# Kernel tuning notes

Measured on AMD Instinct MI355X. Metric: run time of the kernel, lower is better.

## Reference

```python
import jax, jax.numpy as jnp
import numpy as np
import itertools

B, N, K, G = 1024, 1024, 6, 720  # G = K!
H1, H2, C = 64, 32, 40
IN = K * 3


def setup_inputs() -> dict:
    key = jax.random.key(0)
    ks = jax.random.split(key, 8)
    x = jax.random.normal(ks[0], (B, N, 3), dtype=jnp.float32)
    # per-sample subsample indices (torch uses randperm(N)[:K]; distinctness
    # is irrelevant to the math, randint keeps them in-range)
    idx = jax.random.randint(ks[1], (B, K), 0, N)
    perms = jnp.asarray(
        np.array(list(itertools.permutations(range(K))), dtype=np.int32)
    )  # (G, K)
    # MLP params: torch Linear default init ~ U(-1/sqrt(fan_in), 1/sqrt(fan_in))
    def lin(k, fin, fout):
        kw, kb = jax.random.split(k)
        s = 1.0 / np.sqrt(fin)
        W = jax.random.uniform(kw, (fin, fout), jnp.float32, -s, s)
        b = jax.random.uniform(kb, (fout,), jnp.float32, -s, s)
        return W, b
    W1, b1 = lin(ks[2], IN, H1)
    W2, b2 = lin(ks[3], H1, H2)
    W3, b3 = lin(ks[4], H2, C)
    return dict(x=x, W1=W1, b1=b1, W2=W2, b2=b2, W3=W3, b3=b3,
                idx=idx, perms=perms)


def reference(x, W1, b1, W2, b2, W3, b3, idx, perms):
    Bv = x.shape[0]
    Gv, Kv = perms.shape
    # gather the K subsampled points per batch element: (B, K, 3)
    pts = jnp.take_along_axis(x, idx[:, :, None], axis=1)
    # expand over all K! permutations of the point ordering: (B, G, K, 3)
    permuted = pts[:, perms, :]
    flat = permuted.reshape(Bv, Gv, Kv * 3)  # (B, G, K*3)
    h = jax.nn.relu(flat @ W1 + b1)          # (B, G, H1)
    h = jax.nn.relu(h @ W2 + b2)             # (B, G, H2)
    y = h @ W3 + b3                          # (B, G, C)
    return y.mean(axis=1)                    # (B, C)
```

## Files before the change

kernel.cpp:

```cpp
#include <hip/hip_runtime.h>
#include <hip/hip_bf16.h>

typedef __attribute__((ext_vector_type(8))) short short8;
typedef __attribute__((ext_vector_type(4))) float f32x4;
typedef __attribute__((ext_vector_type(4))) unsigned int u32x4;
typedef __attribute__((ext_vector_type(2))) unsigned int u32x2;

#define NN 1024

#define LFENCE { asm volatile("s_waitcnt lgkmcnt(0)" ::: "memory"); __builtin_amdgcn_sched_barrier(0); }

#define ROW_W(BUF, ROW, VAL) { \
  float v_ = fmaxf((VAL), 0.0f); \
  __hip_bfloat16 hb_ = __float2bfloat16(v_); \
  BUF[((ROW) * 64) + (lane ^ ((((ROW)) & 7) << 3))] = *(short*)&hb_; \
}

#define ROW6(BUF, R, BX) \
  ROW_W(BUF,(R)+0,(BX)+T0_) ROW_W(BUF,(R)+1,(BX)+T1_) ROW_W(BUF,(R)+2,(BX)+T2_) \
  ROW_W(BUF,(R)+3,(BX)+T3_) ROW_W(BUF,(R)+4,(BX)+T4_) ROW_W(BUF,(R)+5,(BX)+T5_)

#define SGR(BUF, A0,A1,A2, M0,M1,M2) do { \
  const float f0_ = b1v + P[(A0)*6+0]; \
  const float f1_ = b1v + P[(A1)*6+0]; \
  const float f2_ = b1v + P[(A2)*6+0]; \
  const float g12_ = P[(A1)*6+1] + P[(A2)*6+2]; \
  const float g21_ = P[(A2)*6+1] + P[(A1)*6+2]; \
  const float g02_ = P[(A0)*6+1] + P[(A2)*6+2]; \
  const float g20_ = P[(A2)*6+1] + P[(A0)*6+2]; \
  const float g01_ = P[(A0)*6+1] + P[(A1)*6+2]; \
  const float g10_ = P[(A1)*6+1] + P[(A0)*6+2]; \
  const float e0_ = P[(M0)*6+3], e1_ = P[(M1)*6+3], e2_ = P[(M2)*6+3]; \
  const float h12_ = P[(M1)*6+4] + P[(M2)*6+5]; \
  const float h21_ = P[(M2)*6+4] + P[(M1)*6+5]; \
  const float h02_ = P[(M0)*6+4] + P[(M2)*6+5]; \
  const float h20_ = P[(M2)*6+4] + P[(M0)*6+5]; \
  const float h01_ = P[(M0)*6+4] + P[(M1)*6+5]; \
  const float h10_ = P[(M1)*6+4] + P[(M0)*6+5]; \
  const float T0_ = e0_+h12_, T1_ = e0_+h21_, T2_ = e1_+h02_; \
  const float T3_ = e1_+h20_, T4_ = e2_+h01_, T5_ = e2_+h10_; \
  const float B0_ = f0_+g12_, B1_ = f0_+g21_, B2_ = f1_+g02_; \
  const float B3_ = f1_+g20_, B4_ = f2_+g01_, B5_ = f2_+g10_; \
  ROW6(BUF, 0,  B0_) ROW6(BUF, 6,  B1_) ROW6(BUF, 12, B2_) \
  ROW6(BUF, 18, B3_) ROW6(BUF, 24, B4_) ROW6(BUF, 30, B5_) \
} while(0)

#define MFMA4T(A0_, A1_) do { \
  f32x4 c0_ = {b2v0,b2v0,b2v0,b2v0}; \
  f32x4 c1_ = {b2v1,b2v1,b2v1,b2v1}; \
  c0_ = __builtin_amdgcn_mfma_f32_16x16x32_bf16(A0_, bh00, c0_, 0,0,0); \
  c0_ = __builtin_amdgcn_mfma_f32_16x16x32_bf16(A1_, bh10, c0_, 0,0,0); \
  c1_ = __builtin_amdgcn_mfma_f32_16x16x32_bf16(A0_, bh01, c1_, 0,0,0); \
  c1_ = __builtin_amdgcn_mfma_f32_16x16x32_bf16(A1_, bh11, c1_, 0,0,0); \
  acc0[0]+=fmaxf(c0_[0],0.f); acc0[1]+=fmaxf(c0_[1],0.f); \
  acc0[2]+=fmaxf(c0_[2],0.f); acc0[3]+=fmaxf(c0_[3],0.f); \
  acc1[0]+=fmaxf(c1_[0],0.f); acc1[1]+=fmaxf(c1_[1],0.f); \
  acc1[2]+=fmaxf(c1_[2],0.f); acc1[3]+=fmaxf(c1_[3],0.f); \
} while(0)

#define READS(BUF) { \
  r0 = *(const short8*)&BUF[0*1024 + e0i]; r1 = *(const short8*)&BUF[0*1024 + e1i]; \
  r2 = *(const short8*)&BUF[1*1024 + e0i]; r3 = *(const short8*)&BUF[1*1024 + e1i]; \
  r4 = *(const short8*)&BUF[2*1024 + e0i]; r5 = *(const short8*)&BUF[2*1024 + e1i]; }

#define MFMA3 { MFMA4T(r0,r1); MFMA4T(r2,r3); MFMA4T(r4,r5); }

#define CHUNK(BUF, A0,A1,A2, M0,M1,M2) { SGR(BUF, A0,A1,A2, M0,M1,M2); READS(BUF); LFENCE; }

#define ALLCHUNKS \
    if (wv == 0) { \
        CHUNK(wb0, 0,1,2, 3,4,5); \
        MFMA3; CHUNK(wb1, 0,1,3, 2,4,5); \
        MFMA3; CHUNK(wb0, 0,1,4, 2,3,5); \
        MFMA3; CHUNK(wb1, 0,1,5, 2,3,4); \
        MFMA3; CHUNK(wb0, 0,2,3, 1,4,5); \
        MFMA3; \
    } else if (wv == 1) { \
        CHUNK(wb0, 0,2,4, 1,3,5); \
        MFMA3; CHUNK(wb1, 0,2,5, 1,3,4); \
        MFMA3; CHUNK(wb0, 0,3,4, 1,2,5); \
        MFMA3; CHUNK(wb1, 0,3,5, 1,2,4); \
        MFMA3; CHUNK(wb0, 0,4,5, 1,2,3); \
        MFMA3; \
    } else if (wv == 2) { \
        CHUNK(wb0, 1,2,3, 0,4,5); \
        MFMA3; CHUNK(wb1, 1,2,4, 0,3,5); \
        MFMA3; CHUNK(wb0, 1,2,5, 0,3,4); \
        MFMA3; CHUNK(wb1, 1,3,4, 0,2,5); \
        MFMA3; CHUNK(wb0, 1,3,5, 0,2,4); \
        MFMA3; \
    } else { \
        CHUNK(wb0, 1,4,5, 0,2,3); \
        MFMA3; CHUNK(wb1, 2,3,4, 0,1,5); \
        MFMA3; CHUNK(wb0, 2,3,5, 0,1,4); \
        MFMA3; CHUNK(wb1, 2,4,5, 0,1,3); \
        MFMA3; CHUNK(wb0, 3,4,5, 0,1,2); \
        MFMA3; \
    }

#define MKB(dst_h, KH, NIDX) do { \
  _Pragma("unroll") \
  for (int e_ = 0; e_ < 8; ++e_) { \
    float f_ = W2[((KH)*32 + kg*8 + e_)*32 + 16*(NIDX) + colb]; \
    __hip_bfloat16 hi_ = __float2bfloat16(f_); \
    dst_h[e_] = *(short*)&hi_; \
  } \
} while(0)

__global__ __launch_bounds__(256, 2) void symm_mlp_kernel(
    const float* __restrict__ x,
    const float* __restrict__ W1, const float* __restrict__ b1,
    const float* __restrict__ W2, const float* __restrict__ b2,
    const float* __restrict__ W3, const float* __restrict__ b3,
    const int* __restrict__ idx,
    float* __restrict__ out)
{
    __shared__ short h1s[4][2][48 * 64];
    __shared__ float redbuf[4][32];

    const int tid   = threadIdx.x;
    const int lane  = tid & 63;
    const int wv    = tid >> 6;
    const int b0    = blockIdx.x * 2;

    int pidx0[6], pidx1[6];
    #pragma unroll
    for (int k = 0; k < 6; ++k) { pidx0[k] = idx[b0 * 6 + k]; pidx1[k] = idx[(b0 + 1) * 6 + k]; }

    float px0[6][3], px1[6][3];
    #pragma unroll
    for (int k = 0; k < 6; ++k)
        #pragma unroll
        for (int d = 0; d < 3; ++d) {
            px0[k][d] = x[(b0 * NN + pidx0[k]) * 3 + d];
            px1[k][d] = x[((b0 + 1) * NN + pidx1[k]) * 3 + d];
        }

    float w1c[18];
    #pragma unroll
    for (int r = 0; r < 18; ++r) w1c[r] = W1[r * 64 + lane];

    const float b1v = b1[lane];
    const int colb = lane & 15, kg = lane >> 4;
    const float b2v0 = b2[colb];
    const float b2v1 = b2[16 + colb];

    short8 bh00, bh10, bh01, bh11;
    MKB(bh00, 0, 0);
    MKB(bh10, 1, 0);
    MKB(bh01, 0, 1);
    MKB(bh11, 1, 1);

    short* wb0 = &h1s[wv][0][0];
    short* wb1 = &h1s[wv][1][0];
    *reinterpret_cast<u32x4*>(&wb0[2304 + lane * 8]) = u32x4{0u,0u,0u,0u};
    *reinterpret_cast<u32x2*>(&wb0[2816 + lane * 4]) = u32x2{0u,0u};
    *reinterpret_cast<u32x4*>(&wb1[2304 + lane * 8]) = u32x4{0u,0u,0u,0u};
    *reinterpret_cast<u32x2*>(&wb1[2816 + lane * 4]) = u32x2{0u,0u};

    const int Xl  = (lane & 7) << 3;
    const int e0i = (lane & 15) * 64 + ((kg * 8) ^ Xl);
    const int e1i = (lane & 15) * 64 + ((32 + kg * 8) ^ Xl);

    short8 r0, r1, r2, r3, r4, r5;

    #pragma unroll 1
    for (int bi = 0; bi < 2; ++bi) {
        float P[36];
        #pragma unroll
        for (int k = 0; k < 6; ++k) {
            const float x0 = bi ? px1[k][0] : px0[k][0];
            const float x1 = bi ? px1[k][1] : px0[k][1];
            const float x2 = bi ? px1[k][2] : px0[k][2];
            #pragma unroll
            for (int j = 0; j < 6; ++j)
                P[k*6+j] = fmaf(x2, w1c[3*j+2], fmaf(x1, w1c[3*j+1], x0 * w1c[3*j+0]));
        }

        f32x4 acc0 = {0.f,0.f,0.f,0.f}, acc1 = {0.f,0.f,0.f,0.f};

        ALLCHUNKS

        float s0 = acc0[0] + acc0[1] + acc0[2] + acc0[3];
        float s1 = acc1[0] + acc1[1] + acc1[2] + acc1[3];
        s0 += __shfl_xor(s0, 16, 64);  s0 += __shfl_xor(s0, 32, 64);
        s1 += __shfl_xor(s1, 16, 64);  s1 += __shfl_xor(s1, 32, 64);
        s0 -= 60.0f * fmaxf(b2v0, 0.0f);
        s1 -= 60.0f * fmaxf(b2v1, 0.0f);

        __syncthreads();
        if (lane < 16)       redbuf[wv][lane] = s0;
        else if (lane < 32)  redbuf[wv][lane] = s1;
        __syncthreads();

        if (tid < 40) {
            float m[32];
            #pragma unroll
            for (int c = 0; c < 32; ++c)
                m[c] = (redbuf[0][c] + redbuf[1][c] + redbuf[2][c] + redbuf[3][c]) * (1.0f / 720.0f);
            float y = b3[tid];
            #pragma unroll
            for (int c = 0; c < 32; ++c) y = fmaf(m[c], W3[c * 40 + tid], y);
            out[(b0 + bi) * 40 + tid] = y;
        }
    }
}

extern "C" void kernel_launch(void* const* d_in, const int* in_sizes, int n_in,
                              void* d_out, int out_size, void* d_ws, size_t ws_size,
                              hipStream_t stream) {
    const float* x  = (const float*)d_in[0];
    const float* W1 = (const float*)d_in[1];
    const float* b1 = (const float*)d_in[2];
    const float* W2 = (const float*)d_in[3];
    const float* b2 = (const float*)d_in[4];
    const float* W3 = (const float*)d_in[5];
    const float* b3 = (const float*)d_in[6];
    const int* idx   = (const int*)d_in[7];
    float* out = (float*)d_out;

    symm_mlp_kernel<<<512, 256, 0, stream>>>(x, W1, b1, W2, b2, W3, b3, idx, out);
}
```

Measured before the change: 21.96 us.

## Pack bf16 row pairs with cvt_pk, permute fragments, one batch per block

The LDS staging of the first hidden layer now packs two permutation rows per 32-bit word using v_cvt_pk_bf16_f32. This halves the number of ds_write operations and the conversion instructions. MFMA A-fragments are rebuilt from wider u32x4 LDS reads using v_perm byte selects, which adds ALU work on the read side. The kernel also processes one batch element per block with a 1024-block grid instead of two per block, which removes the serial batch loop and one barrier and exposes more parallelism.

Result: faster. 19.05 us (-13.3%).

```diff
diff --git a/kernel.cpp b/kernel.cpp
--- a/kernel.cpp
+++ b/kernel.cpp
@@ -3,22 +3,21 @@
 
 typedef __attribute__((ext_vector_type(8))) short short8;
 typedef __attribute__((ext_vector_type(4))) float f32x4;
+typedef unsigned int u32;
 typedef __attribute__((ext_vector_type(4))) unsigned int u32x4;
-typedef __attribute__((ext_vector_type(2))) unsigned int u32x2;
 
 #define NN 1024
 
 #define LFENCE { asm volatile("s_waitcnt lgkmcnt(0)" ::: "memory"); __builtin_amdgcn_sched_barrier(0); }
 
-#define ROW_W(BUF, ROW, VAL) { \
-  float v_ = fmaxf((VAL), 0.0f); \
-  __hip_bfloat16 hb_ = __float2bfloat16(v_); \
-  BUF[((ROW) * 64) + (lane ^ ((((ROW)) & 7) << 3))] = *(short*)&hb_; \
+#define PAIR_W(BUF, R2, TA, TB) { \
+  float va_ = fmaxf(bx_ + (TA), 0.0f), vb_ = fmaxf(bx_ + (TB), 0.0f); \
+  u32 pk_; asm("v_cvt_pk_bf16_f32 %0, %1, %2" : "=v"(pk_) : "v"(va_), "v"(vb_)); \
+  BUF[(R2)*64 + (lane ^ ((((R2)) & 7) << 3))] = pk_; \
 }
 
-#define ROW6(BUF, R, BX) \
-  ROW_W(BUF,(R)+0,(BX)+T0_) ROW_W(BUF,(R)+1,(BX)+T1_) ROW_W(BUF,(R)+2,(BX)+T2_) \
-  ROW_W(BUF,(R)+3,(BX)+T3_) ROW_W(BUF,(R)+4,(BX)+T4_) ROW_W(BUF,(R)+5,(BX)+T5_)
+#define ROWP3(BUF, R2B, BX) { const float bx_ = (BX); \
+  PAIR_W(BUF,(R2B)+0, T0_, T1_) PAIR_W(BUF,(R2B)+1, T2_, T3_) PAIR_W(BUF,(R2B)+2, T4_, T5_) }
 
 #define SGR(BUF, A0,A1,A2, M0,M1,M2) do { \
   const float f0_ = b1v + P[(A0)*6+0]; \
@@ -41,8 +40,8 @@
   const float T3_ = e1_+h20_, T4_ = e2_+h01_, T5_ = e2_+h10_; \
   const float B0_ = f0_+g12_, B1_ = f0_+g21_, B2_ = f1_+g02_; \
   const float B3_ = f1_+g20_, B4_ = f2_+g01_, B5_ = f2_+g10_; \
-  ROW6(BUF, 0,  B0_) ROW6(BUF, 6,  B1_) ROW6(BUF, 12, B2_) \
-  ROW6(BUF, 18, B3_) ROW6(BUF, 24, B4_) ROW6(BUF, 30, B5_) \
+  ROWP3(BUF, 0,  B0_) ROWP3(BUF, 3,  B1_) ROWP3(BUF, 6,  B2_) \
+  ROWP3(BUF, 9,  B3_) ROWP3(BUF, 12, B4_) ROWP3(BUF, 15, B5_) \
 } while(0)
 
 #define MFMA4T(A0_, A1_) do { \
@@ -58,14 +57,29 @@
   acc1[2]+=fmaxf(c1_[2],0.f); acc1[3]+=fmaxf(c1_[3],0.f); \
 } while(0)
 
-#define READS(BUF) { \
-  r0 = *(const short8*)&BUF[0*1024 + e0i]; r1 = *(const short8*)&BUF[0*1024 + e1i]; \
-  r2 = *(const short8*)&BUF[1*1024 + e0i]; r3 = *(const short8*)&BUF[1*1024 + e1i]; \
-  r4 = *(const short8*)&BUF[2*1024 + e0i]; r5 = *(const short8*)&BUF[2*1024 + e1i]; }
-
-#define MFMA3 { MFMA4T(r0,r1); MFMA4T(r2,r3); MFMA4T(r4,r5); }
-
-#define CHUNK(BUF, A0,A1,A2, M0,M1,M2) { SGR(BUF, A0,A1,A2, M0,M1,M2); READS(BUF); LFENCE; }
+#define READQ(BUF) { \
+  q0  = *(const u32x4*)&BUF[e0b];         q1  = *(const u32x4*)&BUF[e0b+4]; \
+  q2  = *(const u32x4*)&BUF[e1b];         q3  = *(const u32x4*)&BUF[e1b+4]; \
+  q4  = *(const u32x4*)&BUF[512+e0b];     q5  = *(const u32x4*)&BUF[512+e0b+4]; \
+  q6  = *(const u32x4*)&BUF[512+e1b];     q7  = *(const u32x4*)&BUF[512+e1b+4]; \
+  q8  = *(const u32x4*)&BUF[1024+e0b];    q9  = *(const u32x4*)&BUF[1024+e0b+4]; \
+  q10 = *(const u32x4*)&BUF[1024+e1b];    q11 = *(const u32x4*)&BUF[1024+e1b+4]; }
+
+#define FRAG(dst, qa_, qb_) { \
+  u32x4 t_; \
+  t_[0] = __builtin_amdgcn_perm(qa_[1], qa_[0], sel); \
+  t_[1] = __builtin_amdgcn_perm(qa_[3], qa_[2], sel); \
+  t_[2] = __builtin_amdgcn_perm(qb_[1], qb_[0], sel); \
+  t_[3] = __builtin_amdgcn_perm(qb_[3], qb_[2], sel); \
+  dst = __builtin_bit_cast(short8, t_); }
+
+#define MFMA3 { \
+  short8 A0_, A1_; \
+  FRAG(A0_, q0, q1);   FRAG(A1_, q2, q3);   MFMA4T(A0_, A1_); \
+  FRAG(A0_, q4, q5);   FRAG(A1_, q6, q7);   MFMA4T(A0_, A1_); \
+  FRAG(A0_, q8, q9);   FRAG(A1_, q10, q11); MFMA4T(A0_, A1_); }
+
+#define CHUNK(BUF, A0,A1,A2, M0,M1,M2) { SGR(BUF, A0,A1,A2, M0,M1,M2); READQ(BUF); LFENCE; }
 
 #define ALLCHUNKS \
     if (wv == 0) { \
@@ -115,26 +129,23 @@
     const int* __restrict__ idx,
     float* __restrict__ out)
 {
-    __shared__ short h1s[4][2][48 * 64];
+    __shared__ u32 h1s[4][2][24 * 64];
     __shared__ float redbuf[4][32];
 
     const int tid   = threadIdx.x;
     const int lane  = tid & 63;
     const int wv    = tid >> 6;
-    const int b0    = blockIdx.x * 2;
-
-    int pidx0[6], pidx1[6];
-    #pragma unroll
-    for (int k = 0; k < 6; ++k) { pidx0[k] = idx[b0 * 6 + k]; pidx1[k] = idx[(b0 + 1) * 6 + k]; }
-
-    float px0[6][3], px1[6][3];
+    const int batch = blockIdx.x;
+
+    int pidx[6];
+    #pragma unroll
+    for (int k = 0; k < 6; ++k) pidx[k] = idx[batch * 6 + k];
+
+    float px[6][3];
     #pragma unroll
     for (int k = 0; k < 6; ++k)
         #pragma unroll
-        for (int d = 0; d < 3; ++d) {
-            px0[k][d] = x[(b0 * NN + pidx0[k]) * 3 + d];
-            px1[k][d] = x[((b0 + 1) * NN + pidx1[k]) * 3 + d];
-        }
+        for (int d = 0; d < 3; ++d) px[k][d] = x[(batch * NN + pidx[k]) * 3 + d];
 
     float w1c[18];
     #pragma unroll
@@ -151,58 +162,49 @@
     MKB(bh01, 0, 1);
     MKB(bh11, 1, 1);
 
-    short* wb0 = &h1s[wv][0][0];
-    short* wb1 = &h1s[wv][1][0];
-    *reinterpret_cast<u32x4*>(&wb0[2304 + lane * 8]) = u32x4{0u,0u,0u,0u};
-    *reinterpret_cast<u32x2*>(&wb0[2816 + lane * 4]) = u32x2{0u,0u};
-    *reinterpret_cast<u32x4*>(&wb1[2304 + lane * 8]) = u32x4{0u,0u,0u,0u};
-    *reinterpret_cast<u32x2*>(&wb1[2816 + lane * 4]) = u32x2{0u,0u};
-
-    const int Xl  = (lane & 7) << 3;
-    const int e0i = (lane & 15) * 64 + ((kg * 8) ^ Xl);
-    const int e1i = (lane & 15) * 64 + ((32 + kg * 8) ^ Xl);
-
-    short8 r0, r1, r2, r3, r4, r5;
-
-    #pragma unroll 1
-    for (int bi = 0; bi < 2; ++bi) {
-        float P[36];
+    float P[36];
+    #pragma unroll
+    for (int k = 0; k < 6; ++k)
+    #pragma unroll
+    for (int j = 0; j < 6; ++j)
+        P[k*6+j] = fmaf(px[k][2], w1c[3*j+2], fmaf(px[k][1], w1c[3*j+1], px[k][0] * w1c[3*j+0]));
+
+    u32* wb0 = &h1s[wv][0][0];
+    u32* wb1 = &h1s[wv][1][0];
+    #pragma unroll
+    for (int r2p = 18; r2p < 24; ++r2p) { wb0[r2p*64 + lane] = 0u; wb1[r2p*64 + lane] = 0u; }
+
+    const int r2l = (lane & 15) >> 1;
+    const int sm  = r2l << 3;
+    const int e0b = r2l * 64 + ((kg * 8) ^ sm);
+    const int e1b = r2l * 64 + ((32 + kg * 8) ^ sm);
+    const u32 sel = (lane & 1) ? 0x07060302u : 0x05040100u;
+
+    f32x4 acc0 = {0.f,0.f,0.f,0.f}, acc1 = {0.f,0.f,0.f,0.f};
+    u32x4 q0,q1,q2,q3,q4,q5,q6,q7,q8,q9,q10,q11;
+
+    ALLCHUNKS
+
+    float s0 = acc0[0] + acc0[1] + acc0[2] + acc0[3];
+    float s1 = acc1[0] + acc1[1] + acc1[2] + acc1[3];
+    s0 += __shfl_xor(s0, 16, 64);  s0 += __shfl_xor(s0, 32, 64);
+    s1 += __shfl_xor(s1, 16, 64);  s1 += __shfl_xor(s1, 32, 64);
+    s0 -= 60.0f * fmaxf(b2v0, 0.0f);
+    s1 -= 60.0f * fmaxf(b2v1, 0.0f);
+
+    if (lane < 16)       redbuf[wv][lane] = s0;
+    else if (lane < 32)  redbuf[wv][lane] = s1;
+    __syncthreads();
+
+    if (tid < 40) {
+        float m[32];
         #pragma unroll
-        for (int k = 0; k < 6; ++k) {
-            const float x0 = bi ? px1[k][0] : px0[k][0];
-            const float x1 = bi ? px1[k][1] : px0[k][1];
-            const float x2 = bi ? px1[k][2] : px0[k][2];
-            #pragma unroll
-            for (int j = 0; j < 6; ++j)
-                P[k*6+j] = fmaf(x2, w1c[3*j+2], fmaf(x1, w1c[3*j+1], x0 * w1c[3*j+0]));
-        }
-
-        f32x4 acc0 = {0.f,0.f,0.f,0.f}, acc1 = {0.f,0.f,0.f,0.f};
-
-        ALLCHUNKS
-
-        float s0 = acc0[0] + acc0[1] + acc0[2] + acc0[3];
-        float s1 = acc1[0] + acc1[1] + acc1[2] + acc1[3];
-        s0 += __shfl_xor(s0, 16, 64);  s0 += __shfl_xor(s0, 32, 64);
-        s1 += __shfl_xor(s1, 16, 64);  s1 += __shfl_xor(s1, 32, 64);
-        s0 -= 60.0f * fmaxf(b2v0, 0.0f);
-        s1 -= 60.0f * fmaxf(b2v1, 0.0f);
-
-        __syncthreads();
-        if (lane < 16)       redbuf[wv][lane] = s0;
-        else if (lane < 32)  redbuf[wv][lane] = s1;
-        __syncthreads();
-
-        if (tid < 40) {
-            float m[32];
-            #pragma unroll
-            for (int c = 0; c < 32; ++c)
-                m[c] = (redbuf[0][c] + redbuf[1][c] + redbuf[2][c] + redbuf[3][c]) * (1.0f / 720.0f);
-            float y = b3[tid];
-            #pragma unroll
-            for (int c = 0; c < 32; ++c) y = fmaf(m[c], W3[c * 40 + tid], y);
-            out[(b0 + bi) * 40 + tid] = y;
-        }
+        for (int c = 0; c < 32; ++c)
+            m[c] = (redbuf[0][c] + redbuf[1][c] + redbuf[2][c] + redbuf[3][c]) * (1.0f / 720.0f);
+        float y = b3[tid];
+        #pragma unroll
+        for (int c = 0; c < 32; ++c) y = fmaf(m[c], W3[c * 40 + tid], y);
+        out[batch * 40 + tid] = y;
     }
 }
 
@@ -219,5 +221,5 @@
     const int* idx   = (const int*)d_in[7];
     float* out = (float*)d_out;
 
-    symm_mlp_kernel<<<512, 256, 0, stream>>>(x, W1, b1, W2, b2, W3, b3, idx, out);
+    symm_mlp_kernel<<<1024, 256, 0, stream>>>(x, W1, b1, W2, b2, W3, b3, idx, out);
 }
```
